# Kernel tuning notes

Measured on AMD Instinct MI355X. Metric: run time of the kernel, lower is better.

## Reference

```python
import jax, jax.numpy as jnp
import numpy as np

DIM = 1024
NUM_HEADS = 16
DIM_PER_HEAD = 64
INNER = NUM_HEADS * DIM_PER_HEAD  # 1024
SCALE = DIM_PER_HEAD ** -0.5
EPS = 1e-10


def setup_inputs() -> dict:
    key = jax.random.key(0)
    k_x, k_m, k_qkv, k_wo, k_bo = jax.random.split(key, 5)
    b, l = 2, 2048
    x = jax.random.normal(k_x, (b, l, DIM), dtype=jnp.float32)
    # binary multiplicative mask [b, l, l]
    mask = jax.random.randint(k_m, (b, l, l), 0, 2).astype(jnp.float32)
    # nn.Linear(dim, 3*inner, bias=False): weight [3*inner, dim]; we store transposed [dim, 3*inner]
    W_qkv = jax.random.normal(k_qkv, (DIM, 3 * INNER), dtype=jnp.float32) * (DIM ** -0.5)
    W_out = jax.random.normal(k_wo, (INNER, DIM), dtype=jnp.float32) * (INNER ** -0.5)
    b_out = jax.random.normal(k_bo, (DIM,), dtype=jnp.float32) * 0.01
    return {"x": x, "mask": mask, "W_qkv": W_qkv, "W_out": W_out, "b_out": b_out}


def reference(x, mask, W_qkv, W_out, b_out):
    b, l, d = x.shape
    qkv = x @ W_qkv  # [b, l, 3*inner]
    qkv = qkv.reshape(b, l, 3, NUM_HEADS, DIM_PER_HEAD)
    qkv = jnp.transpose(qkv, (2, 0, 3, 1, 4))  # [3, b, h, l, dh]
    q, k, v = qkv[0], qkv[1], qkv[2]
    # softmax FIRST (no additive mask), matching the original module
    attn = jax.nn.softmax(jnp.einsum('bhid,bhjd->bhij', q, k) * SCALE, axis=-1)  # [b,h,l,l]
    # multiplicative mask then renormalize
    attn = attn * mask[:, None, :, :]
    attn = attn / (jnp.sum(attn, axis=-1, keepdims=True) + EPS)
    z = jnp.einsum('bhij,bhjd->bhid', attn, v)  # [b,h,l,dh]
    z = jnp.transpose(z, (0, 2, 1, 3)).reshape(b, l, INNER)
    out = z @ W_out + b_out  # dropout p=0 -> identity
    return out
```

## Files before the change

kernel.cpp:

```cpp
#include <hip/hip_runtime.h>
#include <hip/hip_bf16.h>

#define BATCH 2
#define SEQ   2048
#define DIM   1024
#define HEADS 16
#define DH    64
#define N_QKV 3072
#define M_TOT 4096
#define SCALE 0.125f
#define EPS   1e-10f
#define LOG2E 1.442695041f

typedef __attribute__((ext_vector_type(8))) _Float16 half8;
typedef __attribute__((ext_vector_type(4))) float f32x4;

static __device__ __forceinline__ unsigned short f2h(float f) {
    _Float16 h = (_Float16)f;
    return __builtin_bit_cast(unsigned short, h);
}
static __device__ __forceinline__ unsigned int pkrtz(float a, float b) {
#if defined(__has_builtin) && __has_builtin(__builtin_amdgcn_cvt_pkrtz)
    return __builtin_bit_cast(unsigned int, __builtin_amdgcn_cvt_pkrtz(a, b));
#else
    return (unsigned int)f2h(a) | ((unsigned int)f2h(b) << 16);
#endif
}
static __device__ __forceinline__ void glds16(const void* g, void* l) {
    __builtin_amdgcn_global_load_lds((const __attribute__((address_space(1))) void*)g,
                                     (__attribute__((address_space(3))) void*)l,
                                     16, 0, 0);
}

__global__ __launch_bounds__(256) void prepass(const float* __restrict__ x,
                                               unsigned short* __restrict__ xh,
                                               const float* __restrict__ Wq,
                                               unsigned short* __restrict__ WqT,
                                               const float* __restrict__ Wo,
                                               unsigned short* __restrict__ WoT,
                                               const float* __restrict__ mask,
                                               unsigned short* __restrict__ mbits) {
    const int bid = blockIdx.x;
    const int t   = threadIdx.x;
    __shared__ float tile[32][33];
    __shared__ unsigned char flags[16][256];

    if (bid < 4096) {
        const int i = bid * 256 + t;
        float4 v = reinterpret_cast<const float4*>(x)[i];
        uint2 o;
        o.x = pkrtz(v.x, v.y);
        o.y = pkrtz(v.z, v.w);
        reinterpret_cast<uint2*>(xh)[i] = o;
    } else if (bid < 8192) {
        const float* src; unsigned short* th; int rows, cols, bx;
        if (bid < 7168) { src = Wq; th = WqT; rows = 1024; cols = 3072; bx = bid - 4096;
        } else          { src = Wo; th = WoT; rows = 1024; cols = 1024; bx = bid - 7168; }
        const int nbx = cols / 32;
        const int c0 = (bx % nbx) * 32, r0 = (bx / nbx) * 32;
        const int tx = t & 31, ty = t >> 5;
        #pragma unroll
        for (int i = ty; i < 32; i += 8)
            tile[i][tx] = src[(long)(r0 + i) * cols + c0 + tx];
        __syncthreads();
        #pragma unroll
        for (int i = ty; i < 32; i += 8)
            th[(long)(c0 + i) * rows + r0 + tx] = f2h(tile[tx][i]);
    } else {
        const int bx = bid - 8192;
        const int it = bx & 127;
        const int bb = bx >> 7;
        const int R0 = it * 16;
        const int tl = t >> 6, ln = t & 63;
        for (int c0 = 0; c0 < SEQ; c0 += 256) {
            #pragma unroll
            for (int rr = 0; rr < 16; ++rr)
                flags[rr][t] = mask[((long)bb * SEQ + R0 + rr) * SEQ + c0 + t] != 0.f;
            __syncthreads();
            unsigned int bits = 0;
            #pragma unroll
            for (int nt = 0; nt < 4; ++nt)
                #pragma unroll
                for (int r = 0; r < 4; ++r)
                    bits |= (unsigned int)flags[ln & 15][tl * 64 + nt * 16 + ((ln >> 4) << 2) + r]
                            << (nt * 4 + r);
            mbits[(((long)bb * 128 + it) * 32 + (c0 >> 6) + tl) * 64 + ln] = (unsigned short)bits;
            __syncthreads();
        }
    }
}

__global__ __launch_bounds__(256, 8) void gemm_qkv_f16(
    const unsigned short* __restrict__ Ahg, const unsigned short* __restrict__ Bhg,
    unsigned short* __restrict__ qb, unsigned short* __restrict__ kb,
    unsigned short* __restrict__ vtb) {
    __shared__ __align__(16) unsigned short As[64 * 64];
    __shared__ __align__(16) unsigned short Bs[64 * 64];

    const int n0   = blockIdx.x * 64;
    const int m0   = blockIdx.y * 64;
    const int wave = threadIdx.x >> 6;
    const int lane = threadIdx.x & 63;
    const int l16  = lane & 15;
    const int g    = lane >> 4;
    const int wm   = wave & 1;
    const int wn   = wave >> 1;
    const int sw   = l16 & 7;

    const int sr8 = lane >> 3;
    const int scg = (lane & 7) ^ sr8;

    f32x4 acc[2][2] = {};

    for (int k0 = 0; k0 < DIM; k0 += 64) {
        #pragma unroll
        for (int i = 0; i < 2; ++i) {
            const int row = wave * 16 + i * 8;
            glds16(Ahg + (long)(m0 + row + sr8) * DIM + k0 + scg * 8, &As[row * 64]);
            glds16(Bhg + (long)(n0 + row + sr8) * DIM + k0 + scg * 8, &Bs[row * 64]);
        }
        __syncthreads();

        half8 a[2][2];
        #pragma unroll
        for (int mt = 0; mt < 2; ++mt) {
            const int rbase = (wm * 32 + mt * 16 + l16) * 64;
            #pragma unroll
            for (int kc = 0; kc < 2; ++kc)
                a[mt][kc] = *reinterpret_cast<const half8*>(
                    &As[rbase + (((kc * 4 + g) ^ sw) * 8)]);
        }
        #pragma unroll
        for (int nt = 0; nt < 2; ++nt) {
            const int rbase = (wn * 32 + nt * 16 + l16) * 64;
            const half8 b0 = *reinterpret_cast<const half8*>(&Bs[rbase + (((0 + g) ^ sw) * 8)]);
            const half8 b1 = *reinterpret_cast<const half8*>(&Bs[rbase + (((4 + g) ^ sw) * 8)]);
            #pragma unroll
            for (int mt = 0; mt < 2; ++mt) {
                acc[mt][nt] = __builtin_amdgcn_mfma_f32_16x16x32_f16(a[mt][0], b0, acc[mt][nt], 0, 0, 0);
                acc[mt][nt] = __builtin_amdgcn_mfma_f32_16x16x32_f16(a[mt][1], b1, acc[mt][nt], 0, 0, 0);
            }
        }
        __syncthreads();
    }

    #pragma unroll
    for (int nt = 0; nt < 2; ++nt) {
        const int n     = n0 + wn * 32 + nt * 16 + l16;
        const int which = n >> 10;
        const int rem   = n & 1023;
        const int head  = rem >> 6;
        const int d     = rem & 63;
        #pragma unroll
        for (int mt = 0; mt < 2; ++mt) {
            #pragma unroll
            for (int r = 0; r < 4; ++r) {
                const int m  = m0 + wm * 32 + mt * 16 + g * 4 + r;
                const int bb = m >> 11;
                const int li = m & 2047;
                const int bh_i = bb * HEADS + head;
                const float val = acc[mt][nt][r];
                if (which == 0)
                    qb[((long)bh_i * SEQ + li) * DH + d] = f2h(val * (SCALE * LOG2E));
                else if (which == 1)
                    kb[((long)bh_i * SEQ + li) * DH + d] = f2h(val);
                else
                    vtb[((long)bh_i * DH + d) * SEQ + li] = f2h(val);
            }
        }
    }
}

__global__ __launch_bounds__(256, 4) void gemm_out_f16(
    const unsigned short* __restrict__ Ahg, const unsigned short* __restrict__ Bhg,
    const float* __restrict__ bias, float* __restrict__ out) {
    __shared__ __align__(16) unsigned short As[64 * 64];
    __shared__ __align__(16) unsigned short Bs[64 * 64];

    const int n0   = blockIdx.x * 64;
    const int m0   = blockIdx.y * 64;
    const int wave = threadIdx.x >> 6;
    const int lane = threadIdx.x & 63;
    const int l16  = lane & 15;
    const int g    = lane >> 4;
    const int wm   = wave & 1;
    const int wn   = wave >> 1;
    const int sw   = l16 & 7;

    const int sr8 = lane >> 3;
    const int scg = (lane & 7) ^ sr8;

    f32x4 acc[2][2] = {};

    for (int k0 = 0; k0 < DIM; k0 += 64) {
        #pragma unroll
        for (int i = 0; i < 2; ++i) {
            const int row = wave * 16 + i * 8;
            glds16(Ahg + (long)(m0 + row + sr8) * DIM + k0 + scg * 8, &As[row * 64]);
            glds16(Bhg + (long)(n0 + row + sr8) * DIM + k0 + scg * 8, &Bs[row * 64]);
        }
        __syncthreads();

        half8 a[2][2];
        #pragma unroll
        for (int mt = 0; mt < 2; ++mt) {
            const int rbase = (wm * 32 + mt * 16 + l16) * 64;
            #pragma unroll
            for (int kc = 0; kc < 2; ++kc)
                a[mt][kc] = *reinterpret_cast<const half8*>(
                    &As[rbase + (((kc * 4 + g) ^ sw) * 8)]);
        }
        #pragma unroll
        for (int nt = 0; nt < 2; ++nt) {
            const int rbase = (wn * 32 + nt * 16 + l16) * 64;
            const half8 b0 = *reinterpret_cast<const half8*>(&Bs[rbase + (((0 + g) ^ sw) * 8)]);
            const half8 b1 = *reinterpret_cast<const half8*>(&Bs[rbase + (((4 + g) ^ sw) * 8)]);
            #pragma unroll
            for (int mt = 0; mt < 2; ++mt) {
                acc[mt][nt] = __builtin_amdgcn_mfma_f32_16x16x32_f16(a[mt][0], b0, acc[mt][nt], 0, 0, 0);
                acc[mt][nt] = __builtin_amdgcn_mfma_f32_16x16x32_f16(a[mt][1], b1, acc[mt][nt], 0, 0, 0);
            }
        }
        __syncthreads();
    }

    #pragma unroll
    for (int nt = 0; nt < 2; ++nt) {
        const int n  = n0 + wn * 32 + nt * 16 + l16;
        const float bv = bias[n];
        #pragma unroll
        for (int mt = 0; mt < 2; ++mt) {
            #pragma unroll
            for (int r = 0; r < 4; ++r) {
                const int m = m0 + wm * 32 + mt * 16 + g * 4 + r;
                out[(long)m * DIM + n] = acc[mt][nt][r] + bv;
            }
        }
    }
}

__global__ __launch_bounds__(512, 6) void attn_mfma(const unsigned short* __restrict__ qb,
                                                    const unsigned short* __restrict__ kb,
                                                    const unsigned short* __restrict__ vtb,
                                                    const unsigned short* __restrict__ mbits,
                                                    unsigned short* __restrict__ zh) {
    const int qt   = blockIdx.x;
    const int h    = blockIdx.y;
    const int bb   = blockIdx.z;
    const int bh   = bb * HEADS + h;
    const int wave = threadIdx.x >> 6;
    const int lane = threadIdx.x & 63;
    const int l16  = lane & 15;
    const int g    = lane >> 4;
    const int wm   = wave >> 1;
    const int wj   = wave & 1;

    const int myrow0 = qt * 64 + wm * 16;

    __shared__ __align__(16) unsigned short KV[2][2][64 * 64];
    __shared__ __align__(16) unsigned short Ps[8][16 * 64];

    const int sr8 = lane >> 3;
    const int scg = (lane & 7) ^ sr8;
    const int sw  = l16 & 7;

    const unsigned short* qptr = qb + ((long)bh * SEQ + myrow0 + l16) * DH + g * 8;
    const half8 q0 = *reinterpret_cast<const half8*>(qptr);
    const half8 q1 = *reinterpret_cast<const half8*>(qptr + 32);

    half8 ones;
    #pragma unroll
    for (int j = 0; j < 8; ++j) ones[j] = (_Float16)1.0f;

    f32x4 o[4] = {};
    f32x4 oz = {0.f, 0.f, 0.f, 0.f};

    const unsigned short* mb =
        mbits + (((long)bb * 128 + qt * 4 + wm) * 32 + wj * 16) * 64 + lane;
    const long kbase = (long)bh * SEQ * DH;
    const long vbase = (long)bh * DH * SEQ;
    const int  jb    = wj * 1024;

    for (int it = 0; it < 16; ++it) {
        const int j0 = jb + it * 64;
        const unsigned int bits = mb[(long)it * 64];

        #pragma unroll
        for (int i = 0; i < 2; ++i) {
            const int row = wm * 16 + i * 8;
            glds16(kb  + kbase + (long)(j0 + row + sr8) * DH + scg * 8, &KV[wj][0][row * 64]);
            glds16(vtb + vbase + (long)(row + sr8) * SEQ + j0 + scg * 8, &KV[wj][1][row * 64]);
        }
        __syncthreads();

        f32x4 st[4];
        #pragma unroll
        for (int nt = 0; nt < 4; ++nt) {
            const int rbase = (nt * 16 + l16) * 64;
            const half8 k0 = *reinterpret_cast<const half8*>(&KV[wj][0][rbase + ((0 + g) ^ sw) * 8]);
            const half8 k1 = *reinterpret_cast<const half8*>(&KV[wj][0][rbase + (((4 + g) ^ sw) * 8)]);
            f32x4 acc = {0.f, 0.f, 0.f, 0.f};
            acc = __builtin_amdgcn_mfma_f32_16x16x32_f16(k0, q0, acc, 0, 0, 0);
            acc = __builtin_amdgcn_mfma_f32_16x16x32_f16(k1, q1, acc, 0, 0, 0);
            st[nt] = acc;
        }

        #pragma unroll
        for (int nt = 0; nt < 4; ++nt) {
            float pm[4];
            #pragma unroll
            for (int r = 0; r < 4; ++r) {
                const float p = __builtin_amdgcn_exp2f(st[nt][r]);
                pm[r] = ((bits >> (nt * 4 + r)) & 1u) ? p : 0.f;
            }
            uint2 pk;
            pk.x = pkrtz(pm[0], pm[1]);
            pk.y = pkrtz(pm[2], pm[3]);
            *reinterpret_cast<uint2*>(
                &Ps[wave][l16 * 64 + (((2 * nt + (g >> 1)) ^ sw) * 8) + (g & 1) * 4]) = pk;
        }

        const half8 pb0 = *reinterpret_cast<const half8*>(&Ps[wave][l16 * 64 + ((0 + g) ^ sw) * 8]);
        const half8 pb1 = *reinterpret_cast<const half8*>(&Ps[wave][l16 * 64 + (((4 + g) ^ sw) * 8)]);
        #pragma unroll
        for (int dt = 0; dt < 4; ++dt) {
            const int vb = (dt * 16 + l16) * 64;
            const half8 v0 = *reinterpret_cast<const half8*>(&KV[wj][1][vb + ((0 + g) ^ sw) * 8]);
            const half8 v1 = *reinterpret_cast<const half8*>(&KV[wj][1][vb + (((4 + g) ^ sw) * 8)]);
            o[dt] = __builtin_amdgcn_mfma_f32_16x16x32_f16(v0, pb0, o[dt], 0, 0, 0);
            o[dt] = __builtin_amdgcn_mfma_f32_16x16x32_f16(v1, pb1, o[dt], 0, 0, 0);
        }
        oz = __builtin_amdgcn_mfma_f32_16x16x32_f16(ones, pb0, oz, 0, 0, 0);
        oz = __builtin_amdgcn_mfma_f32_16x16x32_f16(ones, pb1, oz, 0, 0, 0);
        __syncthreads();
    }

    float* cmb = (float*)&KV[0][0][0];
    const int ci = wm * 16 + l16;
    if (wj == 1) {
        #pragma unroll
        for (int dt = 0; dt < 4; ++dt)
            *reinterpret_cast<f32x4*>(&cmb[ci * 68 + dt * 16 + g * 4]) = o[dt];
        if (g == 0) cmb[4352 + ci] = oz[0];
    }
    __syncthreads();
    if (wj == 0) {
        const float Z   = oz[0] + cmb[4352 + ci];
        const float inv = 1.f / (Z + 1e-30f);
        const long obase = ((long)bb * SEQ + myrow0 + l16) * DIM + h * DH;
        #pragma unroll
        for (int dt = 0; dt < 4; ++dt) {
            const f32x4 oc = *reinterpret_cast<const f32x4*>(&cmb[ci * 68 + dt * 16 + g * 4]);
            uint2 pk;
            pk.x = pkrtz((o[dt][0] + oc[0]) * inv, (o[dt][1] + oc[1]) * inv);
            pk.y = pkrtz((o[dt][2] + oc[2]) * inv, (o[dt][3] + oc[3]) * inv);
            *reinterpret_cast<uint2*>(zh + obase + dt * 16 + g * 4) = pk;
        }
    }
}

extern "C" void kernel_launch(void* const* d_in, const int* in_sizes, int n_in,
                              void* d_out, int out_size, void* d_ws, size_t ws_size,
                              hipStream_t stream) {
    const float* x     = (const float*)d_in[0];
    const float* mask  = (const float*)d_in[1];
    const float* W_qkv = (const float*)d_in[2];
    const float* W_out = (const float*)d_in[3];
    const float* b_out = (const float*)d_in[4];
    float* out = (float*)d_out;

    unsigned short* ws = (unsigned short*)d_ws;
    unsigned short* xh    = ws;
    unsigned short* WqT   = xh    + 4194304;
    unsigned short* WoT   = WqT   + 3145728;
    unsigned short* qbu   = WoT   + 1048576;
    unsigned short* kbu   = qbu   + 4194304;
    unsigned short* vtb   = kbu   + 4194304;
    unsigned short* mbits = vtb   + 4194304;
    unsigned short* zz    = xh;

    prepass<<<8448, 256, 0, stream>>>(x, xh, W_qkv, WqT, W_out, WoT, mask, mbits);

    gemm_qkv_f16<<<dim3(48, 64), 256, 0, stream>>>(xh, WqT, qbu, kbu, vtb);

    attn_mfma<<<dim3(SEQ / 64, HEADS, BATCH), 512, 0, stream>>>(qbu, kbu, vtb, mbits, zz);

    gemm_out_f16<<<dim3(16, 64), 256, 0, stream>>>(zz, WoT, b_out, out);
}
```

Measured before the change: 239.2 us.

## Register-prefetch next K tile in QKV GEMM and attention loops

Replaces direct global-to-LDS loads with register prefetching in both the QKV GEMM and the attention kernel. The next tile is loaded into registers while the current tile is computed, then stored to LDS between two barriers, so global latency overlaps with MFMA work. The GEMM's launch-bounds occupancy hint drops from 8 to 6 to leave room for the extra registers. This costs more VGPRs, explicit LDS store instructions, and a second barrier per iteration.

```diff
diff --git a/kernel.cpp b/kernel.cpp
--- a/kernel.cpp
+++ b/kernel.cpp
@@ -30,6 +30,13 @@
     __builtin_amdgcn_global_load_lds((const __attribute__((address_space(1))) void*)g,
                                      (__attribute__((address_space(3))) void*)l,
                                      16, 0, 0);
+}
+
+static __device__ __forceinline__ void pipebar() {
+    asm volatile("s_waitcnt lgkmcnt(0)" ::: "memory");
+    __builtin_amdgcn_s_barrier();
+    asm volatile("" ::: "memory");
+    __builtin_amdgcn_sched_barrier(0);
 }
 
 __global__ __launch_bounds__(256) void prepass(const float* __restrict__ x,
@@ -90,7 +97,7 @@
     }
 }
 
-__global__ __launch_bounds__(256, 8) void gemm_qkv_f16(
+__global__ __launch_bounds__(256, 6) void gemm_qkv_f16(
     const unsigned short* __restrict__ Ahg, const unsigned short* __restrict__ Bhg,
     unsigned short* __restrict__ qb, unsigned short* __restrict__ kb,
     unsigned short* __restrict__ vtb) {
@@ -112,14 +119,33 @@
 
     f32x4 acc[2][2] = {};
 
+    uint4 ar[2], br[2];
+    #pragma unroll
+    for (int i = 0; i < 2; ++i) {
+        const int row = wave * 16 + i * 8;
+        ar[i] = *reinterpret_cast<const uint4*>(Ahg + (long)(m0 + row + sr8) * DIM + scg * 8);
+        br[i] = *reinterpret_cast<const uint4*>(Bhg + (long)(n0 + row + sr8) * DIM + scg * 8);
+    }
+
     for (int k0 = 0; k0 < DIM; k0 += 64) {
+        pipebar();
         #pragma unroll
         for (int i = 0; i < 2; ++i) {
             const int row = wave * 16 + i * 8;
-            glds16(Ahg + (long)(m0 + row + sr8) * DIM + k0 + scg * 8, &As[row * 64]);
-            glds16(Bhg + (long)(n0 + row + sr8) * DIM + k0 + scg * 8, &Bs[row * 64]);
-        }
-        __syncthreads();
+            *reinterpret_cast<uint4*>(&As[row * 64 + lane * 8]) = ar[i];
+            *reinterpret_cast<uint4*>(&Bs[row * 64 + lane * 8]) = br[i];
+        }
+        if (k0 + 64 < DIM) {
+            #pragma unroll
+            for (int i = 0; i < 2; ++i) {
+                const int row = wave * 16 + i * 8;
+                ar[i] = *reinterpret_cast<const uint4*>(
+                    Ahg + (long)(m0 + row + sr8) * DIM + k0 + 64 + scg * 8);
+                br[i] = *reinterpret_cast<const uint4*>(
+                    Bhg + (long)(n0 + row + sr8) * DIM + k0 + 64 + scg * 8);
+            }
+        }
+        pipebar();
 
         half8 a[2][2];
         #pragma unroll
@@ -141,7 +167,6 @@
                 acc[mt][nt] = __builtin_amdgcn_mfma_f32_16x16x32_f16(a[mt][1], b1, acc[mt][nt], 0, 0, 0);
             }
         }
-        __syncthreads();
     }
 
     #pragma unroll
@@ -281,17 +306,36 @@
     const long vbase = (long)bh * DH * SEQ;
     const int  jb    = wj * 1024;
 
+    uint4 kr[2], vr[2];
+    #pragma unroll
+    for (int i = 0; i < 2; ++i) {
+        const int row = wm * 16 + i * 8;
+        kr[i] = *reinterpret_cast<const uint4*>(kb + kbase + (long)(jb + row + sr8) * DH + scg * 8);
+        vr[i] = *reinterpret_cast<const uint4*>(vtb + vbase + (long)(row + sr8) * SEQ + jb + scg * 8);
+    }
+
     for (int it = 0; it < 16; ++it) {
-        const int j0 = jb + it * 64;
         const unsigned int bits = mb[(long)it * 64];
 
+        pipebar();
         #pragma unroll
         for (int i = 0; i < 2; ++i) {
             const int row = wm * 16 + i * 8;
-            glds16(kb  + kbase + (long)(j0 + row + sr8) * DH + scg * 8, &KV[wj][0][row * 64]);
-            glds16(vtb + vbase + (long)(row + sr8) * SEQ + j0 + scg * 8, &KV[wj][1][row * 64]);
-        }
-        __syncthreads();
+            *reinterpret_cast<uint4*>(&KV[wj][0][row * 64 + lane * 8]) = kr[i];
+            *reinterpret_cast<uint4*>(&KV[wj][1][row * 64 + lane * 8]) = vr[i];
+        }
+        if (it < 15) {
+            const int j0n = jb + (it + 1) * 64;
+            #pragma unroll
+            for (int i = 0; i < 2; ++i) {
+                const int row = wm * 16 + i * 8;
+                kr[i] = *reinterpret_cast<const uint4*>(
+                    kb + kbase + (long)(j0n + row + sr8) * DH + scg * 8);
+                vr[i] = *reinterpret_cast<const uint4*>(
+                    vtb + vbase + (long)(row + sr8) * SEQ + j0n + scg * 8);
+            }
+        }
+        pipebar();
 
         f32x4 st[4];
         #pragma unroll
@@ -332,8 +376,9 @@
         }
         oz = __builtin_amdgcn_mfma_f32_16x16x32_f16(ones, pb0, oz, 0, 0, 0);
         oz = __builtin_amdgcn_mfma_f32_16x16x32_f16(ones, pb1, oz, 0, 0, 0);
-        __syncthreads();
-    }
+    }
+
+    __syncthreads();
 
     float* cmb = (float*)&KV[0][0][0];
     const int ci = wm * 16 + l16;
```

Result: slower. 514.9 us (+115.2%).
